# Kernel tuning notes

Hardware: AMD Instinct MI355X
Metric: run time of the kernel (lower is better)

The kernel has to match this reference:

```python
import jax, jax.numpy as jnp
import numpy as np

NUM_NODES = 100000
HIDDEN = 128
NUM_EDGES = 800000


def setup_inputs() -> dict:
    key = jax.random.key(0)
    ks = jax.random.split(key, 8)
    s = 1.0 / np.sqrt(HIDDEN)

    def lin_w(k):
        return jax.random.uniform(k, (HIDDEN, HIDDEN), minval=-s, maxval=s, dtype=jnp.float32)

    return {
        "node_id": jnp.arange(NUM_NODES, dtype=jnp.int64) if jax.config.jax_enable_x64 else jnp.arange(NUM_NODES, dtype=jnp.int32),
        "edge_index": jax.random.randint(ks[0], (2, NUM_EDGES), 0, NUM_NODES),
        "emb": jax.random.normal(ks[1], (NUM_NODES, HIDDEN), dtype=jnp.float32),
        "W1l": lin_w(ks[2]), "b1l": jnp.zeros((HIDDEN,), jnp.float32), "W1r": lin_w(ks[3]),
        "W2l": lin_w(ks[4]), "b2l": jnp.zeros((HIDDEN,), jnp.float32), "W2r": lin_w(ks[5]),
        "W3l": lin_w(ks[6]), "b3l": jnp.zeros((HIDDEN,), jnp.float32), "W3r": lin_w(ks[7]),
    }


def reference(node_id, edge_index, emb, W1l, b1l, W1r, W2l, b2l, W2r, W3l, b3l, W3r):
    # x: [N, H] node features from embedding lookup
    x = emb[node_id]
    src, dst = edge_index[0], edge_index[1]

    # in-degree per target node (PyG mean aggregation; zero-degree -> 0 output)
    deg = jax.ops.segment_sum(jnp.ones((NUM_EDGES,), x.dtype), dst, num_segments=NUM_NODES)
    inv_deg = 1.0 / jnp.maximum(deg, 1.0)  # [N]

    def sage_conv(h, Wl, bl, Wr):
        # gather source features [E, H], scatter-sum at targets, then mean
        aggr = jax.ops.segment_sum(h[src], dst, num_segments=NUM_NODES) * inv_deg[:, None]
        # out = lin_l(aggr) + lin_r(h); lin_l has bias, lin_r has none (PyG defaults)
        return aggr @ Wl.T + bl + h @ Wr.T

    x = jax.nn.relu(sage_conv(x, W1l, b1l, W1r))
    # dropout p=0.2 with training=False is identity (eval mode)
    x = jax.nn.relu(sage_conv(x, W2l, b2l, W2r))
    return sage_conv(x, W3l, b3l, W3r)
```

## Files before the change

### kernel.cpp

```cpp
#include <hip/hip_runtime.h>

#define H 128

typedef float v4f __attribute__((ext_vector_type(4)));
typedef short v8s __attribute__((ext_vector_type(8)));


__device__ inline void split_bf16(float x, unsigned short& hi, unsigned short& lo) {
  unsigned u = __builtin_bit_cast(unsigned, x);
  unsigned r = u + 0x7FFF + ((u >> 16) & 1);
  hi = (unsigned short)(r >> 16);
  float hf = __builtin_bit_cast(float, r & 0xFFFF0000u);
  float d = x - hf;
  unsigned ud = __builtin_bit_cast(unsigned, d);
  unsigned rd = ud + 0x7FFF + ((ud >> 16) & 1);
  lo = (unsigned short)(rd >> 16);
}


__global__ void hist_kernel(const int* __restrict__ dst, int* __restrict__ deg, int E) {
  int e = blockIdx.x * 256 + threadIdx.x;
  if (e < E) atomicAdd(&deg[dst[e]], 1);
}

__global__ __launch_bounds__(1024) void scan1_kernel(const int* __restrict__ deg,
                                                     int* __restrict__ incl,
                                                     int* __restrict__ blk_sum, int N) {
  __shared__ int lds[1024];
  int t = threadIdx.x;
  int i = blockIdx.x * 1024 + t;
  int v = (i < N) ? deg[i] : 0;
  lds[t] = v;
  __syncthreads();
  for (int off = 1; off < 1024; off <<= 1) {
    int x = (t >= off) ? lds[t - off] : 0;
    __syncthreads();
    lds[t] += x;
    __syncthreads();
  }
  if (i < N) incl[i] = lds[t];
  if (t == 1023) blk_sum[blockIdx.x] = lds[1023];
}

__global__ void scan2_kernel(const int* __restrict__ blk_sum, int* __restrict__ blk_off, int B) {
  __shared__ int lds[256];
  int t = threadIdx.x;
  int v = (t < B) ? blk_sum[t] : 0;
  lds[t] = v;
  __syncthreads();
  for (int off = 1; off < 256; off <<= 1) {
    int x = (t >= off) ? lds[t - off] : 0;
    __syncthreads();
    lds[t] += x;
    __syncthreads();
  }
  blk_off[t] = lds[t] - v;
}

__global__ void rowstart_kernel(const int* __restrict__ incl, const int* __restrict__ deg,
                                const int* __restrict__ blk_off, int* __restrict__ row_start,
                                int N) {
  int i = blockIdx.x * 256 + threadIdx.x;
  if (i < N) row_start[i] = blk_off[i >> 10] + incl[i] - deg[i];
}

__global__ void fill_kernel(const int* __restrict__ src, const int* __restrict__ dst,
                            const int* __restrict__ row_start, int* __restrict__ cursor,
                            int* __restrict__ csr_src, int E) {
  int e = blockIdx.x * 256 + threadIdx.x;
  if (e < E) {
    int d = dst[e];
    int p = atomicAdd(&cursor[d], 1);
    csr_src[row_start[d] + p] = src[e];
  }
}


__global__ void gather_kernel(const float* __restrict__ emb, const int* __restrict__ node_id,
                              float* __restrict__ h, int N) {
  int i = blockIdx.x * 256 + threadIdx.x;
  if (i < N * 32) {
    int n = i >> 5, q = i & 31;
    ((float4*)h)[(size_t)n * 32 + q] = ((const float4*)emb)[(size_t)node_id[n] * 32 + q];
  }
}


__global__ void wsplit_kernel(const float* __restrict__ W0, const float* __restrict__ W1,
                              const float* __restrict__ W2, const float* __restrict__ W3,
                              const float* __restrict__ W4, const float* __restrict__ W5,
                              unsigned short* __restrict__ hi, unsigned short* __restrict__ lo) {
  int i = blockIdx.x * 256 + threadIdx.x;
  int plane = i >> 12;
  int e = (i & 4095) * 4;
  const float* src = plane == 0 ? W0 : plane == 1 ? W1 : plane == 2 ? W2
                   : plane == 3 ? W3 : plane == 4 ? W4 : W5;
  float4 v = *(const float4*)(src + e);
  float vv[4] = {v.x, v.y, v.z, v.w};
  unsigned short hs[4], ls[4];
#pragma unroll
  for (int k = 0; k < 4; ++k) split_bf16(vv[k], hs[k], ls[k]);
  size_t base = (size_t)plane * 16384 + e;
  *(uint2*)(&hi[base]) = make_uint2((unsigned)hs[0] | ((unsigned)hs[1] << 16),
                                    (unsigned)hs[2] | ((unsigned)hs[3] << 16));
  *(uint2*)(&lo[base]) = make_uint2((unsigned)ls[0] | ((unsigned)ls[1] << 16),
                                    (unsigned)ls[2] | ((unsigned)ls[3] << 16));
}


__global__ __launch_bounds__(256) void aggregate_kernel(const float* __restrict__ h,
                                                        const int* __restrict__ csr_src,
                                                        const int* __restrict__ row_start,
                                                        const int* __restrict__ deg,
                                                        float* __restrict__ aggr, int N) {
  int node = blockIdx.x * 4 + (threadIdx.x >> 6);
  if (node >= N) return;
  int lane = threadIdx.x & 63;
  int half = lane >> 5;
  int c4 = lane & 31;
  const float4* __restrict__ h4 = (const float4*)h;

  int start = row_start[node];
  int d = deg[node];

  float4 acc = make_float4(0.f, 0.f, 0.f, 0.f);
  int e = half;
  for (; e + 2 < d; e += 4) {
    int s0 = csr_src[start + e];
    int s1 = csr_src[start + e + 2];
    float4 v0 = h4[(size_t)s0 * 32 + c4];
    float4 v1 = h4[(size_t)s1 * 32 + c4];
    acc.x += v0.x + v1.x;
    acc.y += v0.y + v1.y;
    acc.z += v0.z + v1.z;
    acc.w += v0.w + v1.w;
  }
  for (; e < d; e += 2) {
    int s = csr_src[start + e];
    float4 v = h4[(size_t)s * 32 + c4];
    acc.x += v.x;
    acc.y += v.y;
    acc.z += v.z;
    acc.w += v.w;
  }

  acc.x += __shfl_xor(acc.x, 32);
  acc.y += __shfl_xor(acc.y, 32);
  acc.z += __shfl_xor(acc.z, 32);
  acc.w += __shfl_xor(acc.w, 32);

  if (half == 0) {
    float inv = 1.0f / fmaxf((float)d, 1.0f);
    ((float4*)aggr)[(size_t)node * 32 + c4] =
        make_float4(acc.x * inv, acc.y * inv, acc.z * inv, acc.w * inv);
  }
}


template <int RELU>
__global__ __launch_bounds__(256) void gemm_mfma(const float* __restrict__ aggr,
                                                 const float* h,
                                                 const unsigned short* __restrict__ Wl_hi,
                                                 const unsigned short* __restrict__ Wl_lo,
                                                 const unsigned short* __restrict__ Wr_hi,
                                                 const unsigned short* __restrict__ Wr_lo,
                                                 const float* __restrict__ bias,
                                                 float* out, int N) {
  __shared__ __align__(16) unsigned short Ah[4096];
  __shared__ __align__(16) unsigned short Al[4096];
  __shared__ __align__(16) unsigned short Wh[4096];
  __shared__ __align__(16) unsigned short Wl_[4096];

  int tid = threadIdx.x;
  int wave = tid >> 6, lane = tid & 63;
  int m = lane & 15, q = lane >> 4;
  int block_row = blockIdx.x * 128;

  v4f acc[16];
#pragma unroll
  for (int t = 0; t < 16; ++t) acc[t] = (v4f){0.f, 0.f, 0.f, 0.f};

  for (int side = 0; side < 2; ++side) {
    const float* X = side ? h : aggr;
    const unsigned short* WH = side ? Wr_hi : Wl_hi;
    const unsigned short* WL = side ? Wr_lo : Wl_lo;

    for (int kb = 0; kb < 4; ++kb) {
      __syncthreads();

#pragma unroll
      for (int p = 0; p < 4; ++p) {
        int s = p * 256 + tid;
        int row = s >> 3;
        int g = s & 7;
        int grow = block_row + row;
        if (grow >= N) grow = N - 1;
        float4 v = *(const float4*)(X + (size_t)grow * H + kb * 32 + g * 4);
        float vv[4] = {v.x, v.y, v.z, v.w};
        unsigned short hs[4], ls[4];
#pragma unroll
        for (int k = 0; k < 4; ++k) split_bf16(vv[k], hs[k], ls[k]);
        int off = (row >> 4) * 512 + (((g >> 1) * 16) + (row & 15)) * 8 + (g & 1) * 4;
        *(uint2*)(&Ah[off]) = make_uint2((unsigned)hs[0] | ((unsigned)hs[1] << 16),
                                         (unsigned)hs[2] | ((unsigned)hs[3] << 16));
        *(uint2*)(&Al[off]) = make_uint2((unsigned)ls[0] | ((unsigned)ls[1] << 16),
                                         (unsigned)ls[2] | ((unsigned)ls[3] << 16));
      }

#pragma unroll
      for (int p = 0; p < 2; ++p) {
        int s = p * 256 + tid;
        int row = s >> 2;
        int g2 = s & 3;
        size_t gsrc = (size_t)row * H + kb * 32 + g2 * 8;
        v8s wh = *(const v8s*)(WH + gsrc);
        v8s wl = *(const v8s*)(WL + gsrc);
        int off = (row >> 4) * 512 + (g2 * 16 + (row & 15)) * 8;
        *(v8s*)(&Wh[off]) = wh;
        *(v8s*)(&Wl_[off]) = wl;
      }

      __syncthreads();

      const v8s* AhF = (const v8s*)Ah;
      const v8s* AlF = (const v8s*)Al;
      const v8s* WhF = (const v8s*)Wh;
      const v8s* WlF = (const v8s*)Wl_;
      v8s ah0 = AhF[(wave * 2 + 0) * 64 + lane];
      v8s ah1 = AhF[(wave * 2 + 1) * 64 + lane];
      v8s al0 = AlF[(wave * 2 + 0) * 64 + lane];
      v8s al1 = AlF[(wave * 2 + 1) * 64 + lane];
#pragma unroll
      for (int c = 0; c < 8; ++c) {
        v8s bh = WhF[c * 64 + lane];
        v8s bl = WlF[c * 64 + lane];
        acc[c] = __builtin_amdgcn_mfma_f32_16x16x32_bf16(ah0, bh, acc[c], 0, 0, 0);
        acc[c] = __builtin_amdgcn_mfma_f32_16x16x32_bf16(al0, bh, acc[c], 0, 0, 0);
        acc[c] = __builtin_amdgcn_mfma_f32_16x16x32_bf16(ah0, bl, acc[c], 0, 0, 0);
        acc[8 + c] = __builtin_amdgcn_mfma_f32_16x16x32_bf16(ah1, bh, acc[8 + c], 0, 0, 0);
        acc[8 + c] = __builtin_amdgcn_mfma_f32_16x16x32_bf16(al1, bh, acc[8 + c], 0, 0, 0);
        acc[8 + c] = __builtin_amdgcn_mfma_f32_16x16x32_bf16(ah1, bl, acc[8 + c], 0, 0, 0);
      }
    }
  }

  float bv[8];
#pragma unroll
  for (int c = 0; c < 8; ++c) bv[c] = bias[c * 16 + m];
#pragma unroll
  for (int tr = 0; tr < 2; ++tr) {
#pragma unroll
    for (int c = 0; c < 8; ++c) {
      v4f a = acc[tr * 8 + c];
#pragma unroll
      for (int i = 0; i < 4; ++i) {
        int row = block_row + wave * 32 + tr * 16 + q * 4 + i;
        if (row < N) {
          float v = a[i] + bv[c];
          if (RELU) v = fmaxf(v, 0.f);
          out[(size_t)row * H + c * 16 + m] = v;
        }
      }
    }
  }
}


extern "C" void kernel_launch(void* const* d_in, const int* in_sizes, int n_in,
                              void* d_out, int out_size, void* d_ws, size_t ws_size,
                              hipStream_t stream) {
  const int* node_id = (const int*)d_in[0];
  const int* edge_index = (const int*)d_in[1];
  const float* emb = (const float*)d_in[2];
  const float* W1l = (const float*)d_in[3];
  const float* b1l = (const float*)d_in[4];
  const float* W1r = (const float*)d_in[5];
  const float* W2l = (const float*)d_in[6];
  const float* b2l = (const float*)d_in[7];
  const float* W2r = (const float*)d_in[8];
  const float* W3l = (const float*)d_in[9];
  const float* b3l = (const float*)d_in[10];
  const float* W3r = (const float*)d_in[11];

  int N = in_sizes[0];
  int E = in_sizes[1] / 2;
  const int* src = edge_index;
  const int* dst = edge_index + E;

  char* w = (char*)d_ws;
  auto alloc = [&](size_t bytes) {
    void* p = (void*)w;
    w += (bytes + 255) & ~(size_t)255;
    return p;
  };
  int* deg = (int*)alloc((size_t)N * 4);
  int* cursor = (int*)alloc((size_t)N * 4);
  int* row_start = (int*)alloc((size_t)N * 4);
  int* incl = (int*)alloc((size_t)N * 4);
  int* blk_sum = (int*)alloc(1024);
  int* blk_off = (int*)alloc(1024);
  int* csr_src = (int*)alloc((size_t)E * 4);
  float* hbuf = (float*)alloc((size_t)N * H * 4);
  float* aggr = (float*)alloc((size_t)N * H * 4);
  unsigned short* whi = (unsigned short*)alloc(6 * 16384 * 2);
  unsigned short* wlo = (unsigned short*)alloc(6 * 16384 * 2);

  hipMemsetAsync(deg, 0, (size_t)N * 4, stream);
  hipMemsetAsync(cursor, 0, (size_t)N * 4, stream);

  hist_kernel<<<(E + 255) / 256, 256, 0, stream>>>(dst, deg, E);
  int SB = (N + 1023) / 1024;
  scan1_kernel<<<SB, 1024, 0, stream>>>(deg, incl, blk_sum, N);
  scan2_kernel<<<1, 256, 0, stream>>>(blk_sum, blk_off, SB);
  rowstart_kernel<<<(N + 255) / 256, 256, 0, stream>>>(incl, deg, blk_off, row_start, N);
  fill_kernel<<<(E + 255) / 256, 256, 0, stream>>>(src, dst, row_start, cursor, csr_src, E);

  gather_kernel<<<(N * 32 + 255) / 256, 256, 0, stream>>>(emb, node_id, hbuf, N);
  wsplit_kernel<<<96, 256, 0, stream>>>(W1l, W1r, W2l, W2r, W3l, W3r, whi, wlo);

  int gag = (N + 3) / 4;
  int ggm = (N + 127) / 128;

  aggregate_kernel<<<gag, 256, 0, stream>>>(hbuf, csr_src, row_start, deg, aggr, N);
  gemm_mfma<1><<<ggm, 256, 0, stream>>>(aggr, hbuf, whi + 0 * 16384, wlo + 0 * 16384,
                                        whi + 1 * 16384, wlo + 1 * 16384, b1l, hbuf, N);

  aggregate_kernel<<<gag, 256, 0, stream>>>(hbuf, csr_src, row_start, deg, aggr, N);
  gemm_mfma<1><<<ggm, 256, 0, stream>>>(aggr, hbuf, whi + 2 * 16384, wlo + 2 * 16384,
                                        whi + 3 * 16384, wlo + 3 * 16384, b2l, hbuf, N);

  aggregate_kernel<<<gag, 256, 0, stream>>>(hbuf, csr_src, row_start, deg, aggr, N);
  gemm_mfma<0><<<ggm, 256, 0, stream>>>(aggr, hbuf, whi + 4 * 16384, wlo + 4 * 16384,
                                        whi + 5 * 16384, wlo + 5 * 16384, b3l, (float*)d_out, N);
}
```

Baseline: 519.6 us.

## Store bf16 copy of node features and aggregate neighbours from it

Node features are now also written as bf16 by the gather and gemm epilogues. The aggregation kernel reads the half-size bf16 rows, with 4 edges per wave in parallel, and accumulates in fp32. This halves the bytes moved by the random neighbour gathers, at the cost of extra bf16 stores and reduced precision in the mean aggregation.

```diff
diff --git a/kernel.cpp b/kernel.cpp
--- a/kernel.cpp
+++ b/kernel.cpp
@@ -5,6 +5,12 @@
 typedef float v4f __attribute__((ext_vector_type(4)));
 typedef short v8s __attribute__((ext_vector_type(8)));
 
+
+__device__ inline unsigned short bf16_rne(float x) {
+  unsigned u = __builtin_bit_cast(unsigned, x);
+  unsigned r = u + 0x7FFF + ((u >> 16) & 1);
+  return (unsigned short)(r >> 16);
+}
 
 __device__ inline void split_bf16(float x, unsigned short& hi, unsigned short& lo) {
   unsigned u = __builtin_bit_cast(unsigned, x);
@@ -77,11 +83,14 @@
 
 
 __global__ void gather_kernel(const float* __restrict__ emb, const int* __restrict__ node_id,
-                              float* __restrict__ h, int N) {
+                              float* __restrict__ h, unsigned short* __restrict__ hb, int N) {
   int i = blockIdx.x * 256 + threadIdx.x;
   if (i < N * 32) {
     int n = i >> 5, q = i & 31;
-    ((float4*)h)[(size_t)n * 32 + q] = ((const float4*)emb)[(size_t)node_id[n] * 32 + q];
+    float4 v = ((const float4*)emb)[(size_t)node_id[n] * 32 + q];
+    ((float4*)h)[(size_t)n * 32 + q] = v;
+    unsigned b0 = bf16_rne(v.x), b1 = bf16_rne(v.y), b2 = bf16_rne(v.z), b3 = bf16_rne(v.w);
+    *(uint2*)(hb + (size_t)n * H + q * 4) = make_uint2(b0 | (b1 << 16), b2 | (b3 << 16));
   }
 }
 
@@ -108,7 +117,7 @@
 }
 
 
-__global__ __launch_bounds__(256) void aggregate_kernel(const float* __restrict__ h,
+__global__ __launch_bounds__(256) void aggregate_kernel(const unsigned short* __restrict__ hb,
                                                         const int* __restrict__ csr_src,
                                                         const int* __restrict__ row_start,
                                                         const int* __restrict__ deg,
@@ -116,43 +125,51 @@
   int node = blockIdx.x * 4 + (threadIdx.x >> 6);
   if (node >= N) return;
   int lane = threadIdx.x & 63;
-  int half = lane >> 5;
-  int c4 = lane & 31;
-  const float4* __restrict__ h4 = (const float4*)h;
+  int qe = lane >> 4;
+  int cl = lane & 15;
+  const uint4* __restrict__ h16 = (const uint4*)hb;
 
   int start = row_start[node];
   int d = deg[node];
 
-  float4 acc = make_float4(0.f, 0.f, 0.f, 0.f);
-  int e = half;
-  for (; e + 2 < d; e += 4) {
+  float acc[8] = {0.f, 0.f, 0.f, 0.f, 0.f, 0.f, 0.f, 0.f};
+
+  auto accum = [&](uint4 u) {
+    unsigned uu[4] = {u.x, u.y, u.z, u.w};
+#pragma unroll
+    for (int j = 0; j < 4; ++j) {
+      acc[2 * j] += __builtin_bit_cast(float, uu[j] << 16);
+      acc[2 * j + 1] += __builtin_bit_cast(float, uu[j] & 0xFFFF0000u);
+    }
+  };
+
+  int e = qe;
+  for (; e + 4 < d; e += 8) {
     int s0 = csr_src[start + e];
-    int s1 = csr_src[start + e + 2];
-    float4 v0 = h4[(size_t)s0 * 32 + c4];
-    float4 v1 = h4[(size_t)s1 * 32 + c4];
-    acc.x += v0.x + v1.x;
-    acc.y += v0.y + v1.y;
-    acc.z += v0.z + v1.z;
-    acc.w += v0.w + v1.w;
-  }
-  for (; e < d; e += 2) {
+    int s1 = csr_src[start + e + 4];
+    uint4 u0 = h16[(size_t)s0 * 16 + cl];
+    uint4 u1 = h16[(size_t)s1 * 16 + cl];
+    accum(u0);
+    accum(u1);
+  }
+  for (; e < d; e += 4) {
     int s = csr_src[start + e];
-    float4 v = h4[(size_t)s * 32 + c4];
-    acc.x += v.x;
-    acc.y += v.y;
-    acc.z += v.z;
-    acc.w += v.w;
-  }
-
-  acc.x += __shfl_xor(acc.x, 32);
-  acc.y += __shfl_xor(acc.y, 32);
-  acc.z += __shfl_xor(acc.z, 32);
-  acc.w += __shfl_xor(acc.w, 32);
-
-  if (half == 0) {
-    float inv = 1.0f / fmaxf((float)d, 1.0f);
-    ((float4*)aggr)[(size_t)node * 32 + c4] =
-        make_float4(acc.x * inv, acc.y * inv, acc.z * inv, acc.w * inv);
+    accum(h16[(size_t)s * 16 + cl]);
+  }
+
+#pragma unroll
+  for (int j = 0; j < 8; ++j) {
+    acc[j] += __shfl_xor(acc[j], 16);
+    acc[j] += __shfl_xor(acc[j], 32);
+  }
+
+  float inv = 1.0f / fmaxf((float)d, 1.0f);
+  if (qe == 0) {
+    *(float4*)(aggr + (size_t)node * H + cl * 8) =
+        make_float4(acc[0] * inv, acc[1] * inv, acc[2] * inv, acc[3] * inv);
+  } else if (qe == 1) {
+    *(float4*)(aggr + (size_t)node * H + cl * 8 + 4) =
+        make_float4(acc[4] * inv, acc[5] * inv, acc[6] * inv, acc[7] * inv);
   }
 }
 
@@ -165,7 +182,7 @@
                                                  const unsigned short* __restrict__ Wr_hi,
                                                  const unsigned short* __restrict__ Wr_lo,
                                                  const float* __restrict__ bias,
-                                                 float* out, int N) {
+                                                 float* out, unsigned short* hb_out, int N) {
   __shared__ __align__(16) unsigned short Ah[4096];
   __shared__ __align__(16) unsigned short Al[4096];
   __shared__ __align__(16) unsigned short Wh[4096];
@@ -259,6 +276,7 @@
           float v = a[i] + bv[c];
           if (RELU) v = fmaxf(v, 0.f);
           out[(size_t)row * H + c * 16 + m] = v;
+          if (hb_out) hb_out[(size_t)row * H + c * 16 + m] = bf16_rne(v);
         }
       }
     }
@@ -302,6 +320,7 @@
   int* csr_src = (int*)alloc((size_t)E * 4);
   float* hbuf = (float*)alloc((size_t)N * H * 4);
   float* aggr = (float*)alloc((size_t)N * H * 4);
+  unsigned short* hb = (unsigned short*)alloc((size_t)N * H * 2);
   unsigned short* whi = (unsigned short*)alloc(6 * 16384 * 2);
   unsigned short* wlo = (unsigned short*)alloc(6 * 16384 * 2);
 
@@ -315,21 +334,22 @@
   rowstart_kernel<<<(N + 255) / 256, 256, 0, stream>>>(incl, deg, blk_off, row_start, N);
   fill_kernel<<<(E + 255) / 256, 256, 0, stream>>>(src, dst, row_start, cursor, csr_src, E);
 
-  gather_kernel<<<(N * 32 + 255) / 256, 256, 0, stream>>>(emb, node_id, hbuf, N);
+  gather_kernel<<<(N * 32 + 255) / 256, 256, 0, stream>>>(emb, node_id, hbuf, hb, N);
   wsplit_kernel<<<96, 256, 0, stream>>>(W1l, W1r, W2l, W2r, W3l, W3r, whi, wlo);
 
   int gag = (N + 3) / 4;
   int ggm = (N + 127) / 128;
 
-  aggregate_kernel<<<gag, 256, 0, stream>>>(hbuf, csr_src, row_start, deg, aggr, N);
+  aggregate_kernel<<<gag, 256, 0, stream>>>(hb, csr_src, row_start, deg, aggr, N);
   gemm_mfma<1><<<ggm, 256, 0, stream>>>(aggr, hbuf, whi + 0 * 16384, wlo + 0 * 16384,
-                                        whi + 1 * 16384, wlo + 1 * 16384, b1l, hbuf, N);
-
-  aggregate_kernel<<<gag, 256, 0, stream>>>(hbuf, csr_src, row_start, deg, aggr, N);
+                                        whi + 1 * 16384, wlo + 1 * 16384, b1l, hbuf, hb, N);
+
+  aggregate_kernel<<<gag, 256, 0, stream>>>(hb, csr_src, row_start, deg, aggr, N);
   gemm_mfma<1><<<ggm, 256, 0, stream>>>(aggr, hbuf, whi + 2 * 16384, wlo + 2 * 16384,
-                                        whi + 3 * 16384, wlo + 3 * 16384, b2l, hbuf, N);
-
-  aggregate_kernel<<<gag, 256, 0, stream>>>(hbuf, csr_src, row_start, deg, aggr, N);
+                                        whi + 3 * 16384, wlo + 3 * 16384, b2l, hbuf, hb, N);
+
+  aggregate_kernel<<<gag, 256, 0, stream>>>(hb, csr_src, row_start, deg, aggr, N);
   gemm_mfma<0><<<ggm, 256, 0, stream>>>(aggr, hbuf, whi + 4 * 16384, wlo + 4 * 16384,
-                                        whi + 5 * 16384, wlo + 5 * 16384, b3l, (float*)d_out, N);
-}
+                                        whi + 5 * 16384, wlo + 5 * 16384, b3l, (float*)d_out,
+                                        nullptr, N);
+}
```

New measurement: 470.7 us. -9.4%, faster.
